# Kernel tuning notes

Measured on AMD Instinct MI355X. Metric: run time of the kernel, lower is better.

The kernel has to match this reference:

```python
import jax, jax.numpy as jnp
import numpy as np

# NVFP4 E2M1 representable magnitudes and decision midpoints (round-to-nearest)
_E2M1_GRID = np.array([0.0, 0.5, 1.0, 1.5, 2.0, 3.0, 4.0, 6.0], dtype=np.float32)
_E2M1_MIDS = np.array([0.25, 0.75, 1.25, 1.75, 2.5, 3.5, 5.0], dtype=np.float32)
_BLOCK = 16  # quant_tile_shape=(1,16)


def fake_quant_nvfp4(t):
    """Blockwise (16 contiguous elems) E2M1 fake quant with pow2 scales."""
    shape = t.shape
    v = t.reshape(-1, _BLOCK)                      # [n_blocks, 16]
    amax = jnp.max(jnp.abs(v), axis=-1, keepdims=True)
    # power-of-2 scale so that amax/scale <= 6 (E2M1 max)
    exp = jnp.ceil(jnp.log2(jnp.maximum(amax, jnp.float32(1e-30)) / 6.0))
    scale = jnp.where(amax > 0, jnp.exp2(exp), jnp.float32(1.0))
    u = v / scale
    a = jnp.abs(u)
    grid = jnp.asarray(_E2M1_GRID, dtype=t.dtype)
    mids = jnp.asarray(_E2M1_MIDS, dtype=t.dtype)
    idx = jnp.digitize(a, mids)                    # nearest E2M1 magnitude index
    q = jnp.sign(u) * grid[idx]
    return (q * scale).reshape(shape)


def setup_inputs() -> dict:
    key = jax.random.key(0)
    kx, kw = jax.random.split(key)
    x = jax.random.normal(kx, (32, 256, 64, 64), dtype=jnp.float32)
    w = jax.random.normal(kw, (256, 256, 3, 3), dtype=jnp.float32) * 0.05
    return {"x": x, "w": w}


def reference(x, w):
    qx = fake_quant_nvfp4(x)
    qw = fake_quant_nvfp4(w)
    # conv2d, stride 1, padding 1, no bias, NCHW / OIHW
    return jax.lax.conv_general_dilated(
        qx, qw,
        window_strides=(1, 1),
        padding=((1, 1), (1, 1)),
        dimension_numbers=("NCHW", "OIHW", "NCHW"),
    )
```

## Files before the change

kernel.cpp:

```cpp
#include <hip/hip_runtime.h>
#include <stdint.h>
#include <stddef.h>

typedef __attribute__((ext_vector_type(8))) short short8;
typedef __attribute__((ext_vector_type(4))) float f32x4;

#define N_IMG 32
#define C_IN  256
#define HH    64
#define WW    64
#define O_OUT 256
#define HP    66
#define WP    66

#define QX_ELEMS (N_IMG*HP*WP*C_IN)
#define QX_BYTES ((size_t)QX_ELEMS*2)
#define QW_ELEMS (9*O_OUT*C_IN)


__device__ __forceinline__ float e2m1_mag(float a) {
    return a < 0.25f ? 0.0f
         : a < 0.75f ? 0.5f
         : a < 1.25f ? 1.0f
         : a < 1.75f ? 1.5f
         : a < 2.5f  ? 2.0f
         : a < 3.5f  ? 3.0f
         : a < 5.0f  ? 4.0f : 6.0f;
}

__device__ __forceinline__ void blk_scale2(float amax, float& s, float& inv) {
    float ac = fmaxf(amax, 1e-30f);
    int e;
    float m = frexpf(ac, &e);
    int ex = (m > 0.75f) ? (e - 2) : (e - 3);
    if (amax > 0.0f) { s = ldexpf(1.0f, ex); inv = ldexpf(1.0f, -ex); }
    else             { s = 1.0f; inv = 1.0f; }
}

__device__ __forceinline__ unsigned short to_bf16_bits(float v) {
    union { float f; unsigned int u; } cv; cv.f = v;
    return (unsigned short)(cv.u >> 16);
}

__global__ __launch_bounds__(256) void halo_zero_kernel(unsigned short* __restrict__ qx) {
    int id = blockIdx.x * 256 + threadIdx.x;
    size_t off;
    if (id < 135168) {
        int n = id / 4224, r = id % 4224;
        int h = (r / 2112) * 65;
        int k = r % 2112;
        off = (((size_t)(n*HP + h)) * WP) * C_IN + (size_t)k * 8;
    } else {
        int j = id - 135168;
        int n = j >> 12, r = j & 4095;
        int h = 1 + (r >> 6);
        int w = ((r >> 5) & 1) * 65;
        int k = r & 31;
        off = (((size_t)(n*HP + h)) * WP + w) * C_IN + (size_t)k * 8;
    }
    uint4 z; z.x = z.y = z.z = z.w = 0u;
    *(uint4*)(qx + off) = z;
}

__global__ __launch_bounds__(256) void quant_x_kernel(const float* __restrict__ x,
                                                      unsigned short* __restrict__ qx) {
    __shared__ float xf[64][65];
    __shared__ float sarr[4][65];
    __shared__ float iarr[4][65];

    const int bid = blockIdx.x;
    const int n  = bid >> 8;
    const int h  = (bid >> 2) & 63;
    const int cb = bid & 3;
    const int t  = threadIdx.x;

    {
        const int rb = t >> 4;
        const int w4 = (t & 15) * 4;
        const float* src = x + (((size_t)(n*C_IN + cb*64)) * HH + h) * WW;
#pragma unroll
        for (int it = 0; it < 4; ++it) {
            int r = it * 16 + rb;
            float4 g = *(const float4*)(src + (size_t)r * (HH*WW) + w4);
            xf[r][w4+0] = g.x; xf[r][w4+1] = g.y; xf[r][w4+2] = g.z; xf[r][w4+3] = g.w;
        }
    }
    __syncthreads();

    {
        const int c = t >> 2, wb = t & 3;
        float amax = 0.f;
#pragma unroll
        for (int j = 0; j < 16; ++j) amax = fmaxf(amax, fabsf(xf[c][wb*16 + j]));
        float s, inv;
        blk_scale2(amax, s, inv);
        sarr[wb][c] = s;
        iarr[wb][c] = inv;
    }
    __syncthreads();

    {
        const int w = t >> 2, cg = (t & 3) * 16, wb = w >> 4;
        unsigned short outv[16];
#pragma unroll
        for (int i = 0; i < 16; ++i) {
            int c = cg + i;
            float v = xf[c][w];
            float q = copysignf(e2m1_mag(fabsf(v) * iarr[wb][c]) * sarr[wb][c], v);
            outv[i] = to_bf16_bits(q);
        }
        unsigned short* dst = qx + (((size_t)(n*HP + h + 1)) * WP + (w + 1)) * C_IN + cb*64 + cg;
        *(uint4*)(dst)     = *(const uint4*)&outv[0];
        *(uint4*)(dst + 8) = *(const uint4*)&outv[8];
    }
}

__global__ __launch_bounds__(256) void quant_w_kernel(const float* __restrict__ w,
                                                      unsigned short* __restrict__ qw) {
    __shared__ unsigned short lq[2304];
    const int o = blockIdx.x;
    const int t = threadIdx.x;
    const float* src = w + (size_t)o * 2304;
    if (t < 144) {
        float v[16];
#pragma unroll
        for (int j = 0; j < 4; ++j) {
            float4 f = ((const float4*)(src + t*16))[j];
            v[j*4+0]=f.x; v[j*4+1]=f.y; v[j*4+2]=f.z; v[j*4+3]=f.w;
        }
        float amax = 0.f;
#pragma unroll
        for (int j = 0; j < 16; ++j) amax = fmaxf(amax, fabsf(v[j]));
        float s, inv;
        blk_scale2(amax, s, inv);
#pragma unroll
        for (int j = 0; j < 16; ++j)
            lq[t*16 + j] = to_bf16_bits(copysignf(e2m1_mag(fabsf(v[j]) * inv) * s, v[j]));
    }
    __syncthreads();
#pragma unroll
    for (int p = 0; p < 9; ++p)
        qw[((size_t)(p*O_OUT + o)) * C_IN + t] = lq[t*9 + p];
}

__device__ __forceinline__ void gld16(void* lds, const void* g) {
    __builtin_amdgcn_global_load_lds(
        (const __attribute__((address_space(1))) unsigned int*)g,
        (__attribute__((address_space(3))) unsigned int*)lds,
        16, 0, 0);
}

__device__ __forceinline__ short8 rd8(const void* p) {
    return *(const short8*)p;
}

#define MFMA16 __builtin_amdgcn_mfma_f32_16x16x32_bf16

#define MM16(I0, A00, A01, A10, A11, B)                                   \
    do {                                                                  \
        _Pragma("unroll")                                                 \
        for (int j = 0; j < 4; ++j) {                                     \
            acc[I0][j]     = MFMA16(A00, B[j][0], acc[I0][j],     0,0,0); \
            acc[I0][j]     = MFMA16(A01, B[j][1], acc[I0][j],     0,0,0); \
            acc[(I0)+1][j] = MFMA16(A10, B[j][0], acc[(I0)+1][j], 0,0,0); \
            acc[(I0)+1][j] = MFMA16(A11, B[j][1], acc[(I0)+1][j], 0,0,0); \
        }                                                                 \
    } while (0)

#define RDQ(D0, D1, D2, D3, Q)                                            \
    D0 = rd8(LA + rA + (2*(Q))*2048   + cA0);                             \
    D1 = rd8(LA + rA + (2*(Q))*2048   + (cA0^64));                        \
    D2 = rd8(LA + rA + (2*(Q)+1)*2048 + cA0);                             \
    D3 = rd8(LA + rA + (2*(Q)+1)*2048 + (cA0^64));

#define PH_OPEN()                                                         \
    __builtin_amdgcn_s_barrier();                                         \
    asm volatile("s_waitcnt lgkmcnt(0)" ::: "memory");                    \
    __builtin_amdgcn_sched_barrier(0);                                    \
    __builtin_amdgcn_s_setprio(1);

#define PH_CLOSE(VM)                                                      \
    __builtin_amdgcn_s_setprio(0);                                        \
    asm volatile("s_waitcnt " VM ::: "memory");                           \
    __builtin_amdgcn_s_barrier();

#define CONV_TILE(TN, LAOFF, BCUR, BNXT)                                  \
    do {                                                                  \
        const int tn  = (TN);                                             \
        const int pn  = tn >> 2;                                          \
        const int qn  = pn / 3;                                           \
        const int dwn = pn - qn * 3;                                      \
        const int cn  = (tn & 3) << 6;                                    \
        const unsigned short* ga = gA + pn * 65536 + cn;                  \
        const unsigned short* gb = gB + (ptrdiff_t)((qn - 1) * WP + (dwn - 1)) * C_IN + cn; \
        const char* LA = Lc + (LAOFF);                                    \
        char* SA = Lc + ((LAOFF) ^ 65536);                                \
        char* SB = SA + 32768;                                            \
        short8 aA0, aA1, aA2, aA3, aB0, aB1, aB2, aB3;                    \
        \
        RDQ(aA0, aA1, aA2, aA3, 0);                                       \
                     \
        gld16(SB + bwb,        gb);                                       \
        gld16(SB + bwb + 8192, gb + 16896);                               \
        PH_OPEN();                                                        \
        RDQ(aB0, aB1, aB2, aB3, 1);                                       \
        MM16(0, aA0, aA1, aA2, aA3, BCUR);                                \
        PH_CLOSE("vmcnt(3)");                                             \
                            \
        gld16(SB + bwb + 16384, gb + 2*16896);                            \
        gld16(SB + bwb + 24576, gb + 3*16896);                            \
        PH_OPEN();                                                        \
        RDQ(aA0, aA1, aA2, aA3, 2);                                       \
        MM16(2, aB0, aB1, aB2, aB3, BCUR);                                \
        PH_CLOSE("vmcnt(4)");                                             \
                            \
        gld16(SA + awb,        ga);                                       \
        gld16(SA + awb + 4096, ga + 8192);                                \
        PH_OPEN();                                                        \
        RDQ(aB0, aB1, aB2, aB3, 3);                                       \
        MM16(4, aA0, aA1, aA2, aA3, BCUR);                                \
        PH_CLOSE("vmcnt(2)");                                             \
          \
        gld16(SA + awb + 8192,  ga + 16384);                              \
        gld16(SA + awb + 12288, ga + 24576);                              \
        PH_OPEN();                                                        \
        _Pragma("unroll")                                                 \
        for (int j = 0; j < 4; ++j) {                                     \
            BNXT[j][0] = rd8(SB + rB + j*2048 + cA0);                     \
            BNXT[j][1] = rd8(SB + rB + j*2048 + (cA0^64));                \
        }                                                                 \
        MM16(6, aB0, aB1, aB2, aB3, BCUR);                                \
        PH_CLOSE("vmcnt(2)");                                             \
    } while (0)

__global__ __launch_bounds__(512) void conv_kernel(const unsigned short* __restrict__ qw,
                                                   const unsigned short* __restrict__ qx,
                                                   float* __restrict__ out) {
    __shared__ unsigned short lds[65536];
    char* Lc = (char*)lds;

    const int tid  = threadIdx.x;
    const int w    = tid >> 6;
    const int lane = tid & 63;
    const int lo16 = lane & 15;
    const int quad = lane >> 4;
    const int wm   = w & 1;
    const int wn   = w >> 1;

    const int id  = blockIdx.x;
    const int idx = id >> 3;
    const int n   = (id & 7) + ((idx >> 4) << 3);
    const int pt  = idx & 15;
    const int h0  = pt * 4;
    const int hw0 = pt * 256;

    const int trow  = tid >> 3;
    const int c_off = ((tid & 7) ^ (trow & 7)) << 3;
    const unsigned short* gB = qx + ((size_t)((n*HP + h0 + 1) * WP + trow + 1)) * C_IN + c_off;
    const int ro0 = trow + ((tid >= 256) ? 96 : 0);
    const unsigned short* gA = qw + (size_t)ro0 * C_IN + c_off;
    const int awb = w * 1024 + ((w < 4) ? 0 : 12288);
    const int bwb = w * 1024;

    const int key = (lo16 & 7) << 4;
    const int cA0 = (quad << 4) ^ key;
    const int rA  = (wm * 128 + lo16) * 128;
    const int rB  = (wn * 64  + lo16) * 128;

    f32x4 acc[8][4];
#pragma unroll
    for (int i = 0; i < 8; ++i)
#pragma unroll
        for (int j = 0; j < 4; ++j)
            acc[i][j] = (f32x4){0.f, 0.f, 0.f, 0.f};

    {
        const unsigned short* ga = gA;
        const unsigned short* gb = gB - 17152;
        char* SA = Lc;
        char* SB = Lc + 32768;
        gld16(SB + bwb,         gb);
        gld16(SB + bwb + 8192,  gb + 16896);
        gld16(SB + bwb + 16384, gb + 2*16896);
        gld16(SB + bwb + 24576, gb + 3*16896);
        gld16(SA + awb,         ga);
        gld16(SA + awb + 4096,  ga + 8192);
        gld16(SA + awb + 8192,  ga + 16384);
        gld16(SA + awb + 12288, ga + 24576);
        asm volatile("s_waitcnt vmcnt(0)" ::: "memory");
        __builtin_amdgcn_s_barrier();
    }

    short8 b0[4][2], b1[4][2];
    {
        const char* LB = Lc + 32768;
#pragma unroll
        for (int j = 0; j < 4; ++j) {
            b0[j][0] = rd8(LB + rB + j*2048 + cA0);
            b0[j][1] = rd8(LB + rB + j*2048 + (cA0^64));
        }
    }

#pragma unroll 1
    for (int tt = 0; tt < 18; ++tt) {
        const int t0 = tt * 2;
        CONV_TILE(t0 + 1, 0, b0, b1);
        CONV_TILE((t0 + 2 < 36) ? (t0 + 2) : 35, 65536, b1, b0);
    }

    asm volatile("s_waitcnt vmcnt(0)" ::: "memory");

#pragma unroll
    for (int i = 0; i < 8; ++i) {
        const int o = wm * 128 + i * 16 + quad * 4;
        float* orow = out + ((size_t)(n * O_OUT + o)) * (HH*WW) + hw0 + wn * 64 + lo16;
#pragma unroll
        for (int j = 0; j < 4; ++j) {
            float* dst = orow + j * 16;
#pragma unroll
            for (int r = 0; r < 4; ++r)
                dst[(size_t)r * (HH*WW)] = acc[i][j][r];
        }
    }
}

extern "C" void kernel_launch(void* const* d_in, const int* in_sizes, int n_in,
                              void* d_out, int out_size, void* d_ws, size_t ws_size,
                              hipStream_t stream) {
    const float* x = (const float*)d_in[0];
    const float* w = (const float*)d_in[1];
    float* out = (float*)d_out;

    unsigned short* qx = (unsigned short*)d_ws;
    unsigned short* qw = (unsigned short*)((char*)d_ws + QX_BYTES);

    halo_zero_kernel<<<dim3(1040), 256, 0, stream>>>(qx);
    quant_x_kernel<<<dim3(N_IMG*HH*4), 256, 0, stream>>>(x, qx);
    quant_w_kernel<<<dim3(O_OUT), 256, 0, stream>>>(w, qw);
    conv_kernel<<<dim3(512), 512, 0, stream>>>(qw, qx, out);
}
```

Before: 350.1 us.

## Quantize x in registers before transpose and prefetch next tile's A fragments

The x-quant kernel now does the blockwise amax and E2M1 rounding in registers straight from global loads. It stages only bf16 results in shared memory for the NCHW to NHWC transpose, and each block loops over four channel groups, so there are four times fewer blocks. In the conv kernel, all four B-tile global loads are issued at the start of each tile, and the first A fragment of the next tile is read from LDS during the last MFMA phase, with vmcnt waits adjusted. This aims to overlap LDS reads with MFMA work and to cut shared-memory traffic in the quant pass, at the cost of more live registers and fewer, longer quant blocks.

```diff
diff --git a/kernel.cpp b/kernel.cpp
--- a/kernel.cpp
+++ b/kernel.cpp
@@ -64,54 +64,47 @@
 
 __global__ __launch_bounds__(256) void quant_x_kernel(const float* __restrict__ x,
                                                       unsigned short* __restrict__ qx) {
-    __shared__ float xf[64][65];
-    __shared__ float sarr[4][65];
-    __shared__ float iarr[4][65];
+    __shared__ unsigned short xq[64][66];
 
     const int bid = blockIdx.x;
-    const int n  = bid >> 8;
-    const int h  = (bid >> 2) & 63;
-    const int cb = bid & 3;
-    const int t  = threadIdx.x;
-
-    {
-        const int rb = t >> 4;
-        const int w4 = (t & 15) * 4;
-        const float* src = x + (((size_t)(n*C_IN + cb*64)) * HH + h) * WW;
-#pragma unroll
-        for (int it = 0; it < 4; ++it) {
-            int r = it * 16 + rb;
-            float4 g = *(const float4*)(src + (size_t)r * (HH*WW) + w4);
-            xf[r][w4+0] = g.x; xf[r][w4+1] = g.y; xf[r][w4+2] = g.z; xf[r][w4+3] = g.w;
-        }
-    }
-    __syncthreads();
-
-    {
-        const int c = t >> 2, wb = t & 3;
+    const int n = bid >> 6;
+    const int h = bid & 63;
+    const int t = threadIdx.x;
+    const int c_l = t >> 2;
+    const int wq  = t & 3;
+    const int wr  = t & 63;
+    const int cg  = (t >> 6) * 16;
+
+    const float* srcb = x + (((size_t)(n*C_IN + c_l)) * HH + h) * WW + wq*16;
+    unsigned short* dstb = qx + (((size_t)(n*HP + h + 1)) * WP + (wr + 1)) * C_IN + cg;
+
+    for (int cb = 0; cb < 4; ++cb) {
+        const float* src = srcb + (size_t)(cb*64) * (HH*WW);
+        float v[16];
+#pragma unroll
+        for (int j = 0; j < 4; ++j) {
+            float4 f = ((const float4*)src)[j];
+            v[j*4+0]=f.x; v[j*4+1]=f.y; v[j*4+2]=f.z; v[j*4+3]=f.w;
+        }
         float amax = 0.f;
 #pragma unroll
-        for (int j = 0; j < 16; ++j) amax = fmaxf(amax, fabsf(xf[c][wb*16 + j]));
+        for (int k = 0; k < 16; ++k) amax = fmaxf(amax, fabsf(v[k]));
         float s, inv;
         blk_scale2(amax, s, inv);
-        sarr[wb][c] = s;
-        iarr[wb][c] = inv;
-    }
-    __syncthreads();
-
-    {
-        const int w = t >> 2, cg = (t & 3) * 16, wb = w >> 4;
+#pragma unroll
+        for (int k = 0; k < 8; ++k) {
+            unsigned short lo = to_bf16_bits(copysignf(e2m1_mag(fabsf(v[2*k])   * inv) * s, v[2*k]));
+            unsigned short hi = to_bf16_bits(copysignf(e2m1_mag(fabsf(v[2*k+1]) * inv) * s, v[2*k+1]));
+            *(unsigned int*)&xq[c_l][wq*16 + 2*k] = ((unsigned int)hi << 16) | (unsigned int)lo;
+        }
+        __syncthreads();
         unsigned short outv[16];
 #pragma unroll
-        for (int i = 0; i < 16; ++i) {
-            int c = cg + i;
-            float v = xf[c][w];
-            float q = copysignf(e2m1_mag(fabsf(v) * iarr[wb][c]) * sarr[wb][c], v);
-            outv[i] = to_bf16_bits(q);
-        }
-        unsigned short* dst = qx + (((size_t)(n*HP + h + 1)) * WP + (w + 1)) * C_IN + cb*64 + cg;
+        for (int i = 0; i < 16; ++i) outv[i] = xq[cg + i][wr];
+        unsigned short* dst = dstb + cb*64;
         *(uint4*)(dst)     = *(const uint4*)&outv[0];
         *(uint4*)(dst + 8) = *(const uint4*)&outv[8];
+        __syncthreads();
     }
 }
 
@@ -167,11 +160,11 @@
         }                                                                 \
     } while (0)
 
-#define RDQ(D0, D1, D2, D3, Q)                                            \
-    D0 = rd8(LA + rA + (2*(Q))*2048   + cA0);                             \
-    D1 = rd8(LA + rA + (2*(Q))*2048   + (cA0^64));                        \
-    D2 = rd8(LA + rA + (2*(Q)+1)*2048 + cA0);                             \
-    D3 = rd8(LA + rA + (2*(Q)+1)*2048 + (cA0^64));
+#define RDQB(D0, D1, D2, D3, BASE, Q)                                     \
+    D0 = rd8((BASE) + rA + (2*(Q))*2048   + cA0);                         \
+    D1 = rd8((BASE) + rA + (2*(Q))*2048   + (cA0^64));                    \
+    D2 = rd8((BASE) + rA + (2*(Q)+1)*2048 + cA0);                         \
+    D3 = rd8((BASE) + rA + (2*(Q)+1)*2048 + (cA0^64));
 
 #define PH_OPEN()                                                         \
     __builtin_amdgcn_s_barrier();                                         \
@@ -196,39 +189,37 @@
         const char* LA = Lc + (LAOFF);                                    \
         char* SA = Lc + ((LAOFF) ^ 65536);                                \
         char* SB = SA + 32768;                                            \
-        short8 aA0, aA1, aA2, aA3, aB0, aB1, aB2, aB3;                    \
-        \
-        RDQ(aA0, aA1, aA2, aA3, 0);                                       \
-                     \
-        gld16(SB + bwb,        gb);                                       \
-        gld16(SB + bwb + 8192, gb + 16896);                               \
-        PH_OPEN();                                                        \
-        RDQ(aB0, aB1, aB2, aB3, 1);                                       \
-        MM16(0, aA0, aA1, aA2, aA3, BCUR);                                \
-        PH_CLOSE("vmcnt(3)");                                             \
-                            \
+         \
+        gld16(SB + bwb,         gb);                                      \
+        gld16(SB + bwb + 8192,  gb + 16896);                              \
         gld16(SB + bwb + 16384, gb + 2*16896);                            \
         gld16(SB + bwb + 24576, gb + 3*16896);                            \
         PH_OPEN();                                                        \
-        RDQ(aA0, aA1, aA2, aA3, 2);                                       \
-        MM16(2, aB0, aB1, aB2, aB3, BCUR);                                \
-        PH_CLOSE("vmcnt(4)");                                             \
-                            \
+        RDQB(aB0, aB1, aB2, aB3, LA, 1);                                  \
+        MM16(0, aA0, aA1, aA2, aA3, BCUR);                                \
+        PH_CLOSE("vmcnt(5)");                                             \
+                   \
         gld16(SA + awb,        ga);                                       \
         gld16(SA + awb + 4096, ga + 8192);                                \
         PH_OPEN();                                                        \
-        RDQ(aB0, aB1, aB2, aB3, 3);                                       \
-        MM16(4, aA0, aA1, aA2, aA3, BCUR);                                \
-        PH_CLOSE("vmcnt(2)");                                             \
-          \
+        RDQB(aA0, aA1, aA2, aA3, LA, 2);                                  \
+        MM16(2, aB0, aB1, aB2, aB3, BCUR);                                \
+        PH_CLOSE("vmcnt(6)");                                             \
+                   \
         gld16(SA + awb + 8192,  ga + 16384);                              \
         gld16(SA + awb + 12288, ga + 24576);                              \
+        PH_OPEN();                                                        \
+        RDQB(aB0, aB1, aB2, aB3, LA, 3);                                  \
+        MM16(4, aA0, aA1, aA2, aA3, BCUR);                                \
+        PH_CLOSE("vmcnt(3)");                                             \
+         \
         PH_OPEN();                                                        \
         _Pragma("unroll")                                                 \
         for (int j = 0; j < 4; ++j) {                                     \
             BNXT[j][0] = rd8(SB + rB + j*2048 + cA0);                     \
             BNXT[j][1] = rd8(SB + rB + j*2048 + (cA0^64));                \
         }                                                                 \
+        RDQB(aA0, aA1, aA2, aA3, SA, 0);                                  \
         MM16(6, aB0, aB1, aB2, aB3, BCUR);                                \
         PH_CLOSE("vmcnt(2)");                                             \
     } while (0)
@@ -291,6 +282,7 @@
         __builtin_amdgcn_s_barrier();
     }
 
+    short8 aA0, aA1, aA2, aA3, aB0, aB1, aB2, aB3;
     short8 b0[4][2], b1[4][2];
     {
         const char* LB = Lc + 32768;
@@ -299,6 +291,8 @@
             b0[j][0] = rd8(LB + rB + j*2048 + cA0);
             b0[j][1] = rd8(LB + rB + j*2048 + (cA0^64));
         }
+        const char* LA = Lc;
+        RDQB(aA0, aA1, aA2, aA3, LA, 0);
     }
 
 #pragma unroll 1
@@ -335,7 +329,7 @@
     unsigned short* qw = (unsigned short*)((char*)d_ws + QX_BYTES);
 
     halo_zero_kernel<<<dim3(1040), 256, 0, stream>>>(qx);
-    quant_x_kernel<<<dim3(N_IMG*HH*4), 256, 0, stream>>>(x, qx);
+    quant_x_kernel<<<dim3(N_IMG*HH), 256, 0, stream>>>(x, qx);
     quant_w_kernel<<<dim3(O_OUT), 256, 0, stream>>>(w, qw);
     conv_kernel<<<dim3(512), 512, 0, stream>>>(qw, qx, out);
 }
```

After: 358.8 us. 1.02x slower.
